# Kernel tuning notes

Measured on AMD Instinct MI355X. Metric: run time of the kernel, lower is better.

## Reference

```python
import jax, jax.numpy as jnp
import numpy as np


def _closest_dist_sum(p1, p2):
    # p1: [B, N, 3], p2: [B, M, 3]
    # Euclidean distance via the expanded quadratic form; matches
    # torch.norm(p1 - p2, 2, dim=3) -> min over p2 -> sum over all.
    d2 = (jnp.sum(p1 * p1, axis=-1)[:, :, None]
          + jnp.sum(p2 * p2, axis=-1)[:, None, :]
          - 2.0 * jnp.einsum('bnd,bmd->bnm', p1, p2))  # [B, N, M]
    d = jnp.sqrt(jnp.maximum(d2, 0.0))
    return jnp.sum(jnp.min(d, axis=2))


def setup_inputs() -> dict:
    key = jax.random.key(0)
    k1, k2 = jax.random.split(key)
    shape_xyz = jax.random.normal(k1, (8, 8192, 6), dtype=jnp.float32)
    skel_xyz = jax.random.normal(k2, (8, 2048, 3), dtype=jnp.float32)
    return {"shape_xyz": shape_xyz, "skel_xyz": skel_xyz}


def reference(shape_xyz, skel_xyz):
    # normals (shape_xyz[:, :, 3:6]) are extracted but unused in the loss
    pts = shape_xyz[:, :, :3]
    cd1 = _closest_dist_sum(pts, skel_xyz)   # shape -> skeleton
    cd2 = _closest_dist_sum(skel_xyz, pts)   # skeleton -> shape
    loss_cd = (cd1 + cd2) * 0.0001
    return loss_cd
```

## Files before the change

kernel.cpp:

```cpp
#include <hip/hip_runtime.h>

#define BATCH   8
#define SHAPE_N 8192
#define SKEL_M  2048
#define CHUNK   1024


typedef short bf16x8 __attribute__((ext_vector_type(8)));
typedef float f32x16 __attribute__((ext_vector_type(16)));
union FragU { bf16x8 v; uint4 u4; };

__device__ __forceinline__ unsigned int f2bf(float a) {
    unsigned int u = __float_as_uint(a);
    return (u + 0x7FFFu + ((u >> 16) & 1u)) >> 16;
}
__device__ __forceinline__ float bf2f(unsigned int h) {
    return __uint_as_float(h << 16);
}
__device__ __forceinline__ unsigned int pack2(unsigned int lo, unsigned int hi) {
    return lo | (hi << 16);
}
__device__ __forceinline__ void bfsplit(float v, unsigned int& h, unsigned int& l) {
    h = f2bf(v);
    l = f2bf(v - bf2f(h));
}

__device__ __forceinline__ void make_bfrag(
    const float* __restrict__ ap, int l, FragU& bf, float& ra)
{
    const float x = ap[0], y = ap[1], z = ap[2];
    ra = x * x + y * y + z * z;
    unsigned int hx, lx, hy, ly, hz, lz;
    bfsplit(x, hx, lx); bfsplit(y, hy, ly); bfsplit(z, hz, lz);
    const unsigned int one = 0x3F80u;
    if (l < 32) {
        bf.u4 = make_uint4(pack2(hx, hy), pack2(hz, one),
                           pack2(lx, ly), pack2(lz, one));
    } else {
        bf.u4 = make_uint4(pack2(hx, hy), pack2(hz, 0u), 0u, 0u);
    }
}

__device__ __forceinline__ float min16(const f32x16& D) {
    const float t0 = fminf(fminf(D[0],  D[1]),  D[2]);
    const float t1 = fminf(fminf(D[3],  D[4]),  D[5]);
    const float t2 = fminf(fminf(D[6],  D[7]),  D[8]);
    const float t3 = fminf(fminf(D[9],  D[10]), D[11]);
    const float t4 = fminf(fminf(D[12], D[13]), D[14]);
    const float u0 = fminf(fminf(t0, t1), t2);
    const float u1 = fminf(fminf(t3, t4), D[15]);
    return fminf(u0, u1);
}

__global__ __launch_bounds__(256) void cd_pack(
    const float* __restrict__ shape, const float* __restrict__ skel,
    uint4* __restrict__ skel_pk, uint4* __restrict__ shape_pk)
{
    const int bid = blockIdx.x, tid = threadIdx.x;
    const float* q;
    uint4* dst;
    int g, r;
    if (bid < 64) {
        const int idx = bid * 256 + tid;
        const int b = idx >> 11, i = idx & 2047;
        q = skel + ((size_t)b * SKEL_M + i) * 3;
        dst = skel_pk + (size_t)b * 4096;
        g = i >> 5; r = i & 31;
    } else {
        const int idx = (bid - 64) * 256 + tid;
        const int b = idx >> 13, i = idx & 8191;
        q = shape + ((size_t)b * SHAPE_N + i) * 6;
        dst = shape_pk + (size_t)b * 16384;
        g = i >> 5; r = i & 31;
    }
    const float bx = q[0], by = q[1], bz = q[2];
    const float cx = -2.f * bx, cy = -2.f * by, cz = -2.f * bz;
    const float rb = bx * bx + by * by + bz * bz;
    unsigned int chx, clx, chy, cly, chz, clz, rbh, rbl;
    bfsplit(cx, chx, clx); bfsplit(cy, chy, cly); bfsplit(cz, chz, clz);
    bfsplit(rb, rbh, rbl);
    dst[g * 64 + r]      = make_uint4(pack2(chx, chy), pack2(chz, rbh),
                                      pack2(chx, chy), pack2(chz, rbl));
    dst[g * 64 + 32 + r] = make_uint4(pack2(clx, cly), pack2(clz, 0u), 0u, 0u);
}

template <int SA>
__device__ __forceinline__ float cd_scan(
    const float* __restrict__ Araw,
    const uint4* __restrict__ pk,
    uint4* sB, float& ra_out)
{
    const int tid = threadIdx.x;
    const int l = tid & 63;

    FragU bf;
    make_bfrag(Araw + (size_t)(l & 31) * SA, l, bf, ra_out);

    const f32x16 Z = {0,0,0,0,0,0,0,0,0,0,0,0,0,0,0,0};
    float rmin = 3.4e38f;
    const unsigned int off0 = (unsigned int)((l >> 5) * 512 + (l & 31) * 16);

    for (int c = 0; c < 2; ++c) {
        __syncthreads();
        const uint4* src = pk + (size_t)c * 2048;
#pragma unroll
        for (int k = 0; k < 2048; k += 256)
            sB[k + tid] = src[k + tid];
        __syncthreads();

        unsigned int o = off0;
#pragma unroll 8
        for (int g = 0; g < CHUNK / 32; ++g) {
            FragU af;
            af.u4 = *(const uint4*)((const char*)sB + o);
            o += 1024;
            f32x16 D = __builtin_amdgcn_mfma_f32_32x32x16_bf16(af.v, bf.v, Z, 0, 0, 0);
            rmin = fminf(rmin, min16(D));
        }
    }
    return fminf(rmin, __shfl_xor(rmin, 32, 64));
}

__global__ __launch_bounds__(256) void cd_main(
    const float* __restrict__ shape, const float* __restrict__ skel,
    const uint4* __restrict__ skel_pk, const uint4* __restrict__ shape_pk,
    float* __restrict__ part1, float* __restrict__ part2)
{
    __shared__ uint4 sB[CHUNK * 2];
    __shared__ float s_wsum[4];
    const int tid = threadIdx.x;
    const int l = tid & 63, wv = tid >> 6;
    const int bid = blockIdx.x;

    if (bid < 512) {
        const int b = bid >> 6, sub = bid & 63;
        float ra;
        const float rmin = cd_scan<6>(
            shape + ((size_t)b * SHAPE_N + sub * 128 + wv * 32) * 6,
            skel_pk + (size_t)b * 4096, sB, ra);
        float d = (l < 32) ? sqrtf(fmaxf(ra + rmin, 0.f)) : 0.f;
        for (int o = 32; o; o >>= 1) d += __shfl_down(d, o, 64);
        if (l == 0) s_wsum[wv] = d;
        __syncthreads();
        if (tid == 0)
            part1[bid] = s_wsum[0] + s_wsum[1] + s_wsum[2] + s_wsum[3];
    } else {
        const int j = bid - 512;
        const int b = j >> 6, rem = j & 63;
        const int asub = rem >> 2, q = rem & 3;
        float ra;
        const float rmin = cd_scan<3>(
            skel + ((size_t)b * SKEL_M + asub * 128 + wv * 32) * 3,
            shape_pk + (size_t)b * 16384 + (size_t)q * 4096, sB, ra);
        if (l < 32)
            part2[(size_t)q * (BATCH * SKEL_M) + b * SKEL_M +
                  asub * 128 + wv * 32 + l] = ra + rmin;
    }
}

__global__ __launch_bounds__(1024) void cd_reduce(
    const float* __restrict__ part1, const float* __restrict__ part2,
    float* __restrict__ out)
{
    __shared__ float s_wsum[16];
    const int t = threadIdx.x;
    float s = 0.f;

    const float4* w4 = (const float4*)part2;
#pragma unroll
    for (int r = 0; r < 4; ++r) {
        const int i4 = r * 1024 + t;
        float4 v0 = w4[i4];
        const float4 v1 = w4[4096 + i4];
        const float4 v2 = w4[8192 + i4];
        const float4 v3 = w4[12288 + i4];
        v0.x = fminf(fminf(v0.x, v1.x), fminf(v2.x, v3.x));
        v0.y = fminf(fminf(v0.y, v1.y), fminf(v2.y, v3.y));
        v0.z = fminf(fminf(v0.z, v1.z), fminf(v2.z, v3.z));
        v0.w = fminf(fminf(v0.w, v1.w), fminf(v2.w, v3.w));
        s += sqrtf(fmaxf(v0.x, 0.f)) + sqrtf(fmaxf(v0.y, 0.f)) +
             sqrtf(fmaxf(v0.z, 0.f)) + sqrtf(fmaxf(v0.w, 0.f));
    }
    if (t < 512) s += part1[t];

    for (int o = 32; o; o >>= 1) s += __shfl_down(s, o, 64);
    const int lane = t & 63, wave = t >> 6;
    if (lane == 0) s_wsum[wave] = s;
    __syncthreads();
    if (t == 0) {
        float tot = 0.f;
#pragma unroll
        for (int w = 0; w < 16; ++w) tot += s_wsum[w];
        out[0] = tot * 1e-4f;
    }
}

extern "C" void kernel_launch(void* const* d_in, const int* in_sizes, int n_in,
                              void* d_out, int out_size, void* d_ws, size_t ws_size,
                              hipStream_t stream) {
    const float* shape = (const float*)d_in[0];
    const float* skel  = (const float*)d_in[1];
    float* out         = (float*)d_out;

    uint4* skel_pk  = (uint4*)d_ws;
    uint4* shape_pk = skel_pk + 32768;
    float* part1    = (float*)(shape_pk + 131072);
    float* part2    = part1 + 512;

    cd_pack<<<320, 256, 0, stream>>>(shape, skel, skel_pk, shape_pk);
    cd_main<<<1024, 256, 0, stream>>>(shape, skel, skel_pk, shape_pk,
                                      part1, part2);
    cd_reduce<<<1, 1024, 0, stream>>>(part1, part2, out);
}
```

Baseline: 76.71 us.

## Fuse final reduction into main kernel via last-block atomic and use direct global-to-LDS loads

Removes the separate single-block reduce launch. Each cd_main block atomically increments a counter that cd_pack resets, and the last block to finish runs the final min/sqrt/sum reduction with 256 threads. The shared-memory staging of packed fragments now uses global_load_lds, so data goes from global memory into LDS without passing through registers. This saves one kernel launch and some register traffic, but adds an atomic and a fence to every block and a serialized tail reduction done by fewer threads.

```diff
diff --git a/kernel.cpp b/kernel.cpp
--- a/kernel.cpp
+++ b/kernel.cpp
@@ -9,6 +9,11 @@
 typedef short bf16x8 __attribute__((ext_vector_type(8)));
 typedef float f32x16 __attribute__((ext_vector_type(16)));
 union FragU { bf16x8 v; uint4 u4; };
+
+#define GL2LDS(gp, lp)                                                  \
+    __builtin_amdgcn_global_load_lds(                                   \
+        (const __attribute__((address_space(1))) unsigned int*)(gp),    \
+        (__attribute__((address_space(3))) unsigned int*)(lp), 16, 0, 0)
 
 __device__ __forceinline__ unsigned int f2bf(float a) {
     unsigned int u = __float_as_uint(a);
@@ -54,9 +59,11 @@
 
 __global__ __launch_bounds__(256) void cd_pack(
     const float* __restrict__ shape, const float* __restrict__ skel,
-    uint4* __restrict__ skel_pk, uint4* __restrict__ shape_pk)
+    uint4* __restrict__ skel_pk, uint4* __restrict__ shape_pk,
+    unsigned int* __restrict__ ctl)
 {
     const int bid = blockIdx.x, tid = threadIdx.x;
+    if (bid == 0 && tid == 0) ctl[0] = 0u;
     const float* q;
     uint4* dst;
     int g, r;
@@ -92,6 +99,7 @@
 {
     const int tid = threadIdx.x;
     const int l = tid & 63;
+    const int wbase = tid & ~63;
 
     FragU bf;
     make_bfrag(Araw + (size_t)(l & 31) * SA, l, bf, ra_out);
@@ -105,7 +113,7 @@
         const uint4* src = pk + (size_t)c * 2048;
 #pragma unroll
         for (int k = 0; k < 2048; k += 256)
-            sB[k + tid] = src[k + tid];
+            GL2LDS(src + k + tid, (char*)sB + (size_t)(k + wbase) * 16);
         __syncthreads();
 
         unsigned int o = off0;
@@ -124,10 +132,12 @@
 __global__ __launch_bounds__(256) void cd_main(
     const float* __restrict__ shape, const float* __restrict__ skel,
     const uint4* __restrict__ skel_pk, const uint4* __restrict__ shape_pk,
-    float* __restrict__ part1, float* __restrict__ part2)
+    float* __restrict__ part1, float* __restrict__ part2,
+    unsigned int* __restrict__ ctl, float* __restrict__ out)
 {
     __shared__ uint4 sB[CHUNK * 2];
     __shared__ float s_wsum[4];
+    __shared__ unsigned int s_last;
     const int tid = threadIdx.x;
     const int l = tid & 63, wv = tid >> 6;
     const int bid = blockIdx.x;
@@ -156,20 +166,19 @@
             part2[(size_t)q * (BATCH * SKEL_M) + b * SKEL_M +
                   asub * 128 + wv * 32 + l] = ra + rmin;
     }
-}
-
-__global__ __launch_bounds__(1024) void cd_reduce(
-    const float* __restrict__ part1, const float* __restrict__ part2,
-    float* __restrict__ out)
-{
-    __shared__ float s_wsum[16];
-    const int t = threadIdx.x;
+
+    __threadfence();
+    __syncthreads();
+    if (tid == 0) s_last = atomicAdd(ctl, 1u);
+    __syncthreads();
+    if (s_last != 1023u) return;
+    __threadfence();
+
     float s = 0.f;
-
     const float4* w4 = (const float4*)part2;
 #pragma unroll
-    for (int r = 0; r < 4; ++r) {
-        const int i4 = r * 1024 + t;
+    for (int r = 0; r < 16; ++r) {
+        const int i4 = r * 256 + tid;
         float4 v0 = w4[i4];
         const float4 v1 = w4[4096 + i4];
         const float4 v2 = w4[8192 + i4];
@@ -181,18 +190,13 @@
         s += sqrtf(fmaxf(v0.x, 0.f)) + sqrtf(fmaxf(v0.y, 0.f)) +
              sqrtf(fmaxf(v0.z, 0.f)) + sqrtf(fmaxf(v0.w, 0.f));
     }
-    if (t < 512) s += part1[t];
+    s += part1[tid] + part1[256 + tid];
 
     for (int o = 32; o; o >>= 1) s += __shfl_down(s, o, 64);
-    const int lane = t & 63, wave = t >> 6;
-    if (lane == 0) s_wsum[wave] = s;
+    if (l == 0) s_wsum[wv] = s;
     __syncthreads();
-    if (t == 0) {
-        float tot = 0.f;
-#pragma unroll
-        for (int w = 0; w < 16; ++w) tot += s_wsum[w];
-        out[0] = tot * 1e-4f;
-    }
+    if (tid == 0)
+        out[0] = (s_wsum[0] + s_wsum[1] + s_wsum[2] + s_wsum[3]) * 1e-4f;
 }
 
 extern "C" void kernel_launch(void* const* d_in, const int* in_sizes, int n_in,
@@ -206,9 +210,9 @@
     uint4* shape_pk = skel_pk + 32768;
     float* part1    = (float*)(shape_pk + 131072);
     float* part2    = part1 + 512;
-
-    cd_pack<<<320, 256, 0, stream>>>(shape, skel, skel_pk, shape_pk);
+    unsigned int* ctl = (unsigned int*)(part2 + 65536);
+
+    cd_pack<<<320, 256, 0, stream>>>(shape, skel, skel_pk, shape_pk, ctl);
     cd_main<<<1024, 256, 0, stream>>>(shape, skel, skel_pk, shape_pk,
-                                      part1, part2);
-    cd_reduce<<<1, 1024, 0, stream>>>(part1, part2, out);
-}
+                                      part1, part2, ctl, out);
+}
```

After: 140.4 us. 1.83x slower.
